# Kernel optimization log

Measured on AMD Instinct MI355X. Metric: run time of the kernel, lower is better.

## Reference

```python
import jax, jax.numpy as jnp
import numpy as np
from jax import lax

B, H, W = 16, 256, 256
NUM_HIDDEN = 12
C = 3 + NUM_HIDDEN + 1  # 16 channels: rgb + hidden + alpha
HID = 64
ALPHA = 1.0
THR = 0.1

SOBEL_X = jnp.array([[-1.0, 0.0, 1.0], [-2.0, 0.0, 2.0], [-1.0, 0.0, 1.0]], jnp.float32) / 8.0
SOBEL_Y = jnp.array([[-1.0, -2.0, -1.0], [0.0, 0.0, 0.0], [1.0, 2.0, 1.0]], jnp.float32) / 8.0


def _sobel_conv(s, k):
    # s: [B,H,W] channel-summed state; k: [3,3]. SAME-padded 2D stencil.
    return lax.conv_general_dilated(
        s[..., None], k[:, :, None, None], window_strides=(1, 1), padding='SAME',
        dimension_numbers=('NHWC', 'HWIO', 'NHWC'))  # [B,H,W,1]


def _alive(x, thr):
    # 3x3 max-pool over alpha channel (index 3), SAME padding.
    a = x[..., 3:4]
    pooled = lax.reduce_window(a, -jnp.inf, lax.max, (1, 3, 3, 1), (1, 1, 1, 1), 'SAME')
    return pooled > thr  # [B,H,W,1] bool


def setup_inputs() -> dict:
    key = jax.random.key(0)
    ks = jax.random.split(key, 7)
    x = jax.random.uniform(ks[0], (B, H, W, C), dtype=jnp.float32)
    # UpdateNet params: 1x1 convs stored as dense matrices [in, out].
    w1 = jax.random.normal(ks[1], (3 * C, HID), dtype=jnp.float32) * (1.0 / np.sqrt(3 * C))
    b1 = jnp.zeros((HID,), jnp.float32)
    w2 = jax.random.normal(ks[2], (HID, HID), dtype=jnp.float32) * (1.0 / np.sqrt(HID))
    b2 = jnp.zeros((HID,), jnp.float32)
    # Original zero-inits w3; use small random values so outputs/grads are nontrivial.
    w3 = jax.random.normal(ks[3], (HID, C), dtype=jnp.float32) * 0.01
    return {'x': x, 'w1': w1, 'b1': b1, 'w2': w2, 'b2': b2, 'w3': w3}


def reference(x, w1, b1, w2, b2, w3):
    pre_life = _alive(x, THR)
    # Sobel perception: kernel[o,i] = sobel for all o,i  =>  each output channel
    # is the sobel filter applied to the channel-sum; broadcast across C channels.
    s = jnp.sum(x, axis=-1)                      # [B,H,W]
    sx = _sobel_conv(s, SOBEL_X)                 # [B,H,W,1]
    sy = _sobel_conv(s, SOBEL_Y)                 # [B,H,W,1]
    perc = jnp.concatenate(
        [x, jnp.broadcast_to(sx, x.shape), jnp.broadcast_to(sy, x.shape)], axis=-1)  # [B,H,W,3C]
    # UpdateNet: two biased 1x1 convs + ReLU, then unbiased 1x1 conv.
    h = jax.nn.relu(jnp.einsum('bhwi,io->bhwo', perc, w1) + b1)
    h = jax.nn.relu(jnp.einsum('bhwi,io->bhwo', h, w2) + b2)
    update = jnp.einsum('bhwi,io->bhwo', h, w3)  # [B,H,W,C]
    # cell_fire_rate == 1.0 -> stochastic update mask is all ones.
    x_new = x + ALPHA * update
    post_life = _alive(x_new, THR)
    life = (pre_life & post_life).astype(x_new.dtype)
    return x_new * life
```

## Files before the change

kernel.cpp:

```cpp
#include <hip/hip_runtime.h>
#include <hip/hip_bf16.h>
#include <cstdint>

#define NPIX (16 * 256 * 256)
#define THRV 0.1f

typedef __bf16 bf16x8 __attribute__((ext_vector_type(8)));
typedef float  f32x4  __attribute__((ext_vector_type(4)));

#define LDS_BARRIER() do {                                    \
    asm volatile("s_waitcnt lgkmcnt(0)" ::: "memory");        \
    __builtin_amdgcn_s_barrier();                             \
} while (0)

#define NSLOT 18

__global__ __launch_bounds__(64) void k_pack(const float* __restrict__ w1,
                                             const float* __restrict__ b1,
                                             const float* __restrict__ w2,
                                             const float* __restrict__ b2,
                                             const float* __restrict__ w3,
                                             float4* __restrict__ wpack) {
    const int lane = threadIdx.x;
    const int r = lane & 15, g = lane >> 4;
#pragma unroll
    for (int n = 0; n < 4; ++n) {
        const int cc = n * 16 + r;
        bf16x8 f;
#pragma unroll
        for (int j = 0; j < 8; ++j) {
            float v = 0.f;
            if (j < 4) v = w1[(g * 4 + j) * 64 + cc];
            else if (g == 0 && j == 4) { for (int t = 0; t < 16; ++t) v += w1[(16 + t) * 64 + cc]; v *= 0.125f; }
            else if (g == 0 && j == 5) { for (int t = 0; t < 16; ++t) v += w1[(32 + t) * 64 + cc]; v *= 0.125f; }
            else if (g == 1 && j == 4) v = b1[cc];
            f[j] = (__bf16)v;
        }
        wpack[n * 64 + lane] = *(const float4*)&f;
    }
#pragma unroll
    for (int s = 0; s < 2; ++s)
#pragma unroll
        for (int n = 0; n < 4; ++n) {
            bf16x8 f;
#pragma unroll
            for (int j = 0; j < 8; ++j) {
                const int psi = (2 * s + (j >> 2)) * 16 + g * 4 + (j & 3);
                f[j] = (__bf16)w2[psi * 64 + n * 16 + r];
            }
            wpack[(4 + s * 4 + n) * 64 + lane] = *(const float4*)&f;
        }
#pragma unroll
    for (int s = 0; s < 2; ++s) {
        bf16x8 f;
#pragma unroll
        for (int j = 0; j < 8; ++j) {
            const int psi = (2 * s + (j >> 2)) * 16 + g * 4 + (j & 3);
            f[j] = (__bf16)w3[psi * 16 + r];
        }
        wpack[(12 + s) * 64 + lane] = *(const float4*)&f;
    }
#pragma unroll
    for (int n = 0; n < 4; ++n) {
        f32x4 v;
#pragma unroll
        for (int q = 0; q < 4; ++q) v[q] = b2[n * 16 + g * 4 + q];
        wpack[(14 + n) * 64 + lane] = *(const float4*)&v;
    }
}

__global__ __launch_bounds__(256, 2) void k_fused(const float* __restrict__ x,
                                                  const float4* __restrict__ wpack,
                                                  float* __restrict__ out,
                                                  unsigned char* __restrict__ rpre,
                                                  unsigned char* __restrict__ anewf) {
    __shared__ float sS[4][256];
    __shared__ float sC3[4][256];

    const int tid = threadIdx.x;
    const int wv = tid >> 6, lane = tid & 63;
    const int r = lane & 15, g = lane >> 4;

    bf16x8 w1f[4], w2f[2][4], w3f[2];
    f32x4 b2v[4];
#pragma unroll
    for (int n = 0; n < 4; ++n) { float4 t = wpack[n * 64 + lane]; w1f[n] = *(bf16x8*)&t; }
#pragma unroll
    for (int s2i = 0; s2i < 2; ++s2i)
#pragma unroll
        for (int n = 0; n < 4; ++n) { float4 t = wpack[(4 + s2i * 4 + n) * 64 + lane]; w2f[s2i][n] = *(bf16x8*)&t; }
#pragma unroll
    for (int s2i = 0; s2i < 2; ++s2i) { float4 t = wpack[(12 + s2i) * 64 + lane]; w3f[s2i] = *(bf16x8*)&t; }
#pragma unroll
    for (int n = 0; n < 4; ++n) { float4 t = wpack[(14 + n) * 64 + lane]; b2v[n] = *(f32x4*)&t; }

    const int swz = (blockIdx.x & 7) * 64 + (blockIdx.x >> 3);
    const int img = swz >> 5;
    const int y0 = (swz & 31) * 8;
    const size_t ibase = (size_t)img << 16;
    const int wcol = wv * 64;
    const int wc = wcol + lane;
    const bool scl = (wc > 0), scr = (wc < 255);

    float4 xf[4], xfA[4], xfN[4];

    auto loadrow = [&](int yl, float4 dst[4]) {
        if ((unsigned)yl < 256u) {
            const size_t rb = ibase + (size_t)yl * 256;
#pragma unroll
            for (int t = 0; t < 4; ++t)
                dst[t] = *(const float4*)(x + (rb + wcol + t * 16 + r) * 16 + g * 4);
        } else {
#pragma unroll
            for (int t = 0; t < 4; ++t) dst[t] = make_float4(0.f, 0.f, 0.f, 0.f);
        }
    };
    auto redwrite = [&](int yl, const float4 src[4]) {
        const int sl = yl & 3;
#pragma unroll
        for (int t = 0; t < 4; ++t) {
            float p = (src[t].x + src[t].y) + (src[t].z + src[t].w);
            p += __shfl_xor(p, 16);
            p += __shfl_xor(p, 32);
            if (g == 0) { sS[sl][wcol + t * 16 + r] = p; sC3[sl][wcol + t * 16 + r] = src[t].w; }
        }
    };

    loadrow(y0 - 1, xfN);
    loadrow(y0, xf);
    loadrow(y0 + 1, xfA);
    redwrite(y0 - 1, xfN);
    redwrite(y0, xf);

#pragma unroll 2
    for (int p = 0; p < 8; ++p) {
        const int y = y0 + p;

        const int yn = (p < 7) ? (y + 2) : 999;
        loadrow(yn, xfN);

        redwrite(y + 1, xfA);
        LDS_BARRIER();

        const float* s0 = sS[(y - 1) & 3];
        const float* s1 = sS[y & 3];
        const float* s2 = sS[(y + 1) & 3];
        const float* c3 = sC3[y & 3];
        const size_t rb = ibase + (size_t)y * 256;

        float gxA, gyA;
        {
            const float r0m = scl ? s0[wc - 1] : 0.f;
            const float r0c = s0[wc];
            const float r0p = scr ? s0[wc + 1] : 0.f;
            const float r1m = scl ? s1[wc - 1] : 0.f;
            const float r1p = scr ? s1[wc + 1] : 0.f;
            const float r2m = scl ? s2[wc - 1] : 0.f;
            const float r2c = s2[wc];
            const float r2p = scr ? s2[wc + 1] : 0.f;
            gxA = (r0p - r0m) + 2.f * (r1p - r1m) + (r2p - r2m);
            gyA = (r2m + 2.f * r2c + r2p) - (r0m + 2.f * r0c + r0p);
            const float c3m = scl ? c3[wc - 1] : 0.f;
            const float c3c = c3[wc];
            const float c3p = scr ? c3[wc + 1] : 0.f;
            rpre[rb + wc] = (fmaxf(c3m, fmaxf(c3c, c3p)) > THRV) ? 1 : 0;
        }

#pragma unroll
        for (int t = 0; t < 4; ++t) {
            const int col = wcol + t * 16 + r;
            const size_t pix = rb + col;
            const float gx = __shfl(gxA, t * 16 + r);
            const float gy = __shfl(gyA, t * 16 + r);

            bf16x8 a1;
            a1[0] = (__bf16)xf[t].x; a1[1] = (__bf16)xf[t].y;
            a1[2] = (__bf16)xf[t].z; a1[3] = (__bf16)xf[t].w;
            a1[4] = (__bf16)(g == 0 ? gx : (g == 1 ? 1.f : 0.f));
            a1[5] = (__bf16)(g == 0 ? gy : 0.f);
            a1[6] = (__bf16)0.f; a1[7] = (__bf16)0.f;

            f32x4 acc1[4];
#pragma unroll
            for (int n = 0; n < 4; ++n)
                acc1[n] = __builtin_amdgcn_mfma_f32_16x16x32_bf16(
                    w1f[n], a1, (f32x4){0.f, 0.f, 0.f, 0.f}, 0, 0, 0);

            bf16x8 bf2[2];
#pragma unroll
            for (int s2i = 0; s2i < 2; ++s2i)
#pragma unroll
                for (int j = 0; j < 4; ++j) {
                    bf2[s2i][j]     = (__bf16)fmaxf(acc1[2 * s2i][j], 0.f);
                    bf2[s2i][4 + j] = (__bf16)fmaxf(acc1[2 * s2i + 1][j], 0.f);
                }

            f32x4 acc2[4];
#pragma unroll
            for (int n = 0; n < 4; ++n) {
                acc2[n] = __builtin_amdgcn_mfma_f32_16x16x32_bf16(w2f[0][n], bf2[0], b2v[n], 0, 0, 0);
                acc2[n] = __builtin_amdgcn_mfma_f32_16x16x32_bf16(w2f[1][n], bf2[1], acc2[n], 0, 0, 0);
            }

            bf16x8 bf3[2];
#pragma unroll
            for (int s2i = 0; s2i < 2; ++s2i)
#pragma unroll
                for (int j = 0; j < 4; ++j) {
                    bf3[s2i][j]     = (__bf16)fmaxf(acc2[2 * s2i][j], 0.f);
                    bf3[s2i][4 + j] = (__bf16)fmaxf(acc2[2 * s2i + 1][j], 0.f);
                }

            f32x4 acc3 = __builtin_amdgcn_mfma_f32_16x16x32_bf16(
                w3f[0], bf3[0], (f32x4){0.f, 0.f, 0.f, 0.f}, 0, 0, 0);
            acc3 = __builtin_amdgcn_mfma_f32_16x16x32_bf16(w3f[1], bf3[1], acc3, 0, 0, 0);

            f32x4 xn;
            xn[0] = xf[t].x + acc3[0]; xn[1] = xf[t].y + acc3[1];
            xn[2] = xf[t].z + acc3[2]; xn[3] = xf[t].w + acc3[3];
            __builtin_nontemporal_store(xn, (f32x4*)(out + pix * 16 + g * 4));
            if (g == 0) anewf[pix] = (xn[3] > THRV) ? 1 : 0;
        }

#pragma unroll
        for (int t = 0; t < 4; ++t) { xf[t] = xfA[t]; xfA[t] = xfN[t]; }
    }
}

__global__ __launch_bounds__(256) void k_post(const unsigned char* __restrict__ rpre,
                                              const unsigned char* __restrict__ anewf,
                                              float* __restrict__ out) {
    const int q = blockIdx.x * 256 + threadIdx.x;
    const int p0 = q * 4;
    const int bi = p0 >> 16;
    const int rem = p0 & 65535;
    const int y = rem >> 8;
    const int c0 = rem & 255;
    const unsigned char* pr = rpre + ((size_t)bi << 16);
    const unsigned char* an = anewf + ((size_t)bi << 16);

    unsigned pre = 0, M = 0, l = 0, rr = 0;
#pragma unroll
    for (int dy = -1; dy <= 1; ++dy) {
        const int y2 = y + dy;
        if ((unsigned)y2 >= 256u) continue;
        const int ro = y2 * 256;
        pre |= *(const unsigned*)(pr + ro + c0);
        M   |= *(const unsigned*)(an + ro + c0);
        l   |= (c0 > 0)   ? (unsigned)an[ro + c0 - 1] : 0u;
        rr  |= (c0 < 252) ? (unsigned)an[ro + c0 + 4] : 0u;
    }
    const unsigned post = M | (M << 8) | l | (M >> 8) | (rr << 24);
    const unsigned alive = pre & post;
    if (alive != 0x01010101u) {
        const f32x4 z = (f32x4){0.f, 0.f, 0.f, 0.f};
#pragma unroll
        for (int i = 0; i < 4; ++i)
            if (!((alive >> (8 * i)) & 1u)) {
                f32x4* op = (f32x4*)(out + (size_t)(p0 + i) * 16);
                op[0] = z; op[1] = z; op[2] = z; op[3] = z;
            }
    }
}

extern "C" void kernel_launch(void* const* d_in, const int* in_sizes, int n_in,
                              void* d_out, int out_size, void* d_ws, size_t ws_size,
                              hipStream_t stream) {
    const float* x  = (const float*)d_in[0];
    const float* w1 = (const float*)d_in[1];
    const float* b1 = (const float*)d_in[2];
    const float* w2 = (const float*)d_in[3];
    const float* b2 = (const float*)d_in[4];
    const float* w3 = (const float*)d_in[5];
    float* out = (float*)d_out;

    unsigned char* rpre  = (unsigned char*)d_ws;
    unsigned char* anewf = rpre + NPIX;
    float4* wpack = (float4*)(anewf + NPIX);

    hipLaunchKernelGGL(k_pack, dim3(1), dim3(64), 0, stream, w1, b1, w2, b2, w3, wpack);
    hipLaunchKernelGGL(k_fused, dim3(512), dim3(256), 0, stream,
                       x, wpack, out, rpre, anewf);
    hipLaunchKernelGGL(k_post, dim3(NPIX / 1024), dim3(256), 0, stream,
                       rpre, anewf, out);
}
```

Before: 42.30 us.

## Split fused kernel into single-wave blocks with halo columns, dropping barriers

Each block becomes one 64-lane wave covering a 64-column by 8-row tile instead of four waves covering full 256-column rows. Neighbouring columns are fetched as per-row halo loads, so the LDS staging rows are wave-private and the per-row workgroup barrier goes away. The grid grows from 512 to 2048 blocks for finer scheduling granularity. The cost is extra halo loads, more weight-register loads per block, and reliance on single-wave LDS ordering without an explicit barrier.

```diff
diff --git a/kernel.cpp b/kernel.cpp
--- a/kernel.cpp
+++ b/kernel.cpp
@@ -7,11 +7,6 @@
 
 typedef __bf16 bf16x8 __attribute__((ext_vector_type(8)));
 typedef float  f32x4  __attribute__((ext_vector_type(4)));
-
-#define LDS_BARRIER() do {                                    \
-    asm volatile("s_waitcnt lgkmcnt(0)" ::: "memory");        \
-    __builtin_amdgcn_s_barrier();                             \
-} while (0)
 
 #define NSLOT 18
 
@@ -69,16 +64,15 @@
     }
 }
 
-__global__ __launch_bounds__(256, 2) void k_fused(const float* __restrict__ x,
-                                                  const float4* __restrict__ wpack,
-                                                  float* __restrict__ out,
-                                                  unsigned char* __restrict__ rpre,
-                                                  unsigned char* __restrict__ anewf) {
-    __shared__ float sS[4][256];
-    __shared__ float sC3[4][256];
-
-    const int tid = threadIdx.x;
-    const int wv = tid >> 6, lane = tid & 63;
+__global__ __launch_bounds__(64) void k_fused(const float* __restrict__ x,
+                                              const float4* __restrict__ wpack,
+                                              float* __restrict__ out,
+                                              unsigned char* __restrict__ rpre,
+                                              unsigned char* __restrict__ anewf) {
+    __shared__ float sS[4][66];
+    __shared__ float sC3[4][66];
+
+    const int lane = threadIdx.x;
     const int r = lane & 15, g = lane >> 4;
 
     bf16x8 w1f[4], w2f[2][4], w3f[2];
@@ -94,43 +88,63 @@
 #pragma unroll
     for (int n = 0; n < 4; ++n) { float4 t = wpack[(14 + n) * 64 + lane]; b2v[n] = *(f32x4*)&t; }
 
-    const int swz = (blockIdx.x & 7) * 64 + (blockIdx.x >> 3);
-    const int img = swz >> 5;
-    const int y0 = (swz & 31) * 8;
+    const int bid = blockIdx.x;
+    const int swz = (bid & 7) * 256 + (bid >> 3);
+    const int img = swz >> 7;
+    const int rem = swz & 127;
+    const int y0 = (rem >> 2) * 8;
+    const int c0 = (rem & 3) * 64;
     const size_t ibase = (size_t)img << 16;
-    const int wcol = wv * 64;
-    const int wc = wcol + lane;
-    const bool scl = (wc > 0), scr = (wc < 255);
-
-    float4 xf[4], xfA[4], xfN[4];
+    const bool hasL = (c0 > 0), hasR = (c0 + 64 < 256);
 
     auto loadrow = [&](int yl, float4 dst[4]) {
         if ((unsigned)yl < 256u) {
             const size_t rb = ibase + (size_t)yl * 256;
 #pragma unroll
             for (int t = 0; t < 4; ++t)
-                dst[t] = *(const float4*)(x + (rb + wcol + t * 16 + r) * 16 + g * 4);
+                dst[t] = *(const float4*)(x + (rb + c0 + t * 16 + r) * 16 + g * 4);
         } else {
 #pragma unroll
             for (int t = 0; t < 4; ++t) dst[t] = make_float4(0.f, 0.f, 0.f, 0.f);
         }
     };
-    auto redwrite = [&](int yl, const float4 src[4]) {
+    auto loadhalo = [&](int yl) -> float4 {
+        float4 h = make_float4(0.f, 0.f, 0.f, 0.f);
+        if (lane < 8 && (unsigned)yl < 256u) {
+            const bool left = (lane < 4);
+            if (left ? hasL : hasR) {
+                const int cc = left ? (c0 - 1) : (c0 + 64);
+                h = *(const float4*)(x + (ibase + (size_t)yl * 256 + cc) * 16 + (lane & 3) * 4);
+            }
+        }
+        return h;
+    };
+    auto redwrite = [&](int yl, const float4 src[4], float4 hch) {
         const int sl = yl & 3;
+        float hv = (hch.x + hch.y) + (hch.z + hch.w);
+        hv += __shfl_xor(hv, 1);
+        hv += __shfl_xor(hv, 2);
 #pragma unroll
         for (int t = 0; t < 4; ++t) {
             float p = (src[t].x + src[t].y) + (src[t].z + src[t].w);
             p += __shfl_xor(p, 16);
             p += __shfl_xor(p, 32);
-            if (g == 0) { sS[sl][wcol + t * 16 + r] = p; sC3[sl][wcol + t * 16 + r] = src[t].w; }
-        }
+            if (g == 0) { sS[sl][1 + t * 16 + r] = p; sC3[sl][1 + t * 16 + r] = src[t].w; }
+        }
+        if (lane == 0) { sS[sl][0]  = hv; sC3[sl][0]  = hch.w; }
+        if (lane == 4) { sS[sl][65] = hv; sC3[sl][65] = hch.w; }
     };
 
-    loadrow(y0 - 1, xfN);
-    loadrow(y0, xf);
-    loadrow(y0 + 1, xfA);
-    redwrite(y0 - 1, xfN);
-    redwrite(y0, xf);
+    float4 xfC[4], xfA[4], xfN[4];
+    float4 hchA;
+    {
+        float4 tmp[4];
+        loadrow(y0 - 1, tmp);  float4 ht = loadhalo(y0 - 1);
+        loadrow(y0, xfC);      float4 h0 = loadhalo(y0);
+        loadrow(y0 + 1, xfA);  hchA = loadhalo(y0 + 1);
+        redwrite(y0 - 1, tmp, ht);
+        redwrite(y0, xfC, h0);
+    }
 
 #pragma unroll 2
     for (int p = 0; p < 8; ++p) {
@@ -138,9 +152,9 @@
 
         const int yn = (p < 7) ? (y + 2) : 999;
         loadrow(yn, xfN);
-
-        redwrite(y + 1, xfA);
-        LDS_BARRIER();
+        float4 hchN = loadhalo(yn);
+
+        redwrite(y + 1, xfA, hchA);
 
         const float* s0 = sS[(y - 1) & 3];
         const float* s1 = sS[y & 3];
@@ -148,34 +162,23 @@
         const float* c3 = sC3[y & 3];
         const size_t rb = ibase + (size_t)y * 256;
 
-        float gxA, gyA;
-        {
-            const float r0m = scl ? s0[wc - 1] : 0.f;
-            const float r0c = s0[wc];
-            const float r0p = scr ? s0[wc + 1] : 0.f;
-            const float r1m = scl ? s1[wc - 1] : 0.f;
-            const float r1p = scr ? s1[wc + 1] : 0.f;
-            const float r2m = scl ? s2[wc - 1] : 0.f;
-            const float r2c = s2[wc];
-            const float r2p = scr ? s2[wc + 1] : 0.f;
-            gxA = (r0p - r0m) + 2.f * (r1p - r1m) + (r2p - r2m);
-            gyA = (r2m + 2.f * r2c + r2p) - (r0m + 2.f * r0c + r0p);
-            const float c3m = scl ? c3[wc - 1] : 0.f;
-            const float c3c = c3[wc];
-            const float c3p = scr ? c3[wc + 1] : 0.f;
-            rpre[rb + wc] = (fmaxf(c3m, fmaxf(c3c, c3p)) > THRV) ? 1 : 0;
-        }
+        const float r0m = s0[lane], r0c = s0[lane + 1], r0p = s0[lane + 2];
+        const float r1m = s1[lane],                     r1p = s1[lane + 2];
+        const float r2m = s2[lane], r2c = s2[lane + 1], r2p = s2[lane + 2];
+        const float gxA = (r0p - r0m) + 2.f * (r1p - r1m) + (r2p - r2m);
+        const float gyA = (r2m + 2.f * r2c + r2p) - (r0m + 2.f * r0c + r0p);
+        const float c3m = c3[lane], c3c = c3[lane + 1], c3p = c3[lane + 2];
+        rpre[rb + c0 + lane] = (fmaxf(c3m, fmaxf(c3c, c3p)) > THRV) ? 1 : 0;
 
 #pragma unroll
         for (int t = 0; t < 4; ++t) {
-            const int col = wcol + t * 16 + r;
-            const size_t pix = rb + col;
+            const size_t pix = rb + c0 + t * 16 + r;
             const float gx = __shfl(gxA, t * 16 + r);
             const float gy = __shfl(gyA, t * 16 + r);
 
             bf16x8 a1;
-            a1[0] = (__bf16)xf[t].x; a1[1] = (__bf16)xf[t].y;
-            a1[2] = (__bf16)xf[t].z; a1[3] = (__bf16)xf[t].w;
+            a1[0] = (__bf16)xfC[t].x; a1[1] = (__bf16)xfC[t].y;
+            a1[2] = (__bf16)xfC[t].z; a1[3] = (__bf16)xfC[t].w;
             a1[4] = (__bf16)(g == 0 ? gx : (g == 1 ? 1.f : 0.f));
             a1[5] = (__bf16)(g == 0 ? gy : 0.f);
             a1[6] = (__bf16)0.f; a1[7] = (__bf16)0.f;
@@ -216,14 +219,15 @@
             acc3 = __builtin_amdgcn_mfma_f32_16x16x32_bf16(w3f[1], bf3[1], acc3, 0, 0, 0);
 
             f32x4 xn;
-            xn[0] = xf[t].x + acc3[0]; xn[1] = xf[t].y + acc3[1];
-            xn[2] = xf[t].z + acc3[2]; xn[3] = xf[t].w + acc3[3];
+            xn[0] = xfC[t].x + acc3[0]; xn[1] = xfC[t].y + acc3[1];
+            xn[2] = xfC[t].z + acc3[2]; xn[3] = xfC[t].w + acc3[3];
             __builtin_nontemporal_store(xn, (f32x4*)(out + pix * 16 + g * 4));
             if (g == 0) anewf[pix] = (xn[3] > THRV) ? 1 : 0;
         }
 
 #pragma unroll
-        for (int t = 0; t < 4; ++t) { xf[t] = xfA[t]; xfA[t] = xfN[t]; }
+        for (int t = 0; t < 4; ++t) { xfC[t] = xfA[t]; xfA[t] = xfN[t]; }
+        hchA = hchN;
     }
 }
 
@@ -279,7 +283,7 @@
     float4* wpack = (float4*)(anewf + NPIX);
 
     hipLaunchKernelGGL(k_pack, dim3(1), dim3(64), 0, stream, w1, b1, w2, b2, w3, wpack);
-    hipLaunchKernelGGL(k_fused, dim3(512), dim3(256), 0, stream,
+    hipLaunchKernelGGL(k_fused, dim3(2048), dim3(64), 0, stream,
                        x, wpack, out, rpre, anewf);
     hipLaunchKernelGGL(k_post, dim3(NPIX / 1024), dim3(256), 0, stream,
                        rpre, anewf, out);
```

Result: slower. 44.24 us (+4.6%).
